# Kernel optimization log

Hardware: AMD Instinct MI355X
Metric: run time of the kernel (lower is better)

## Reference

```python
import jax, jax.numpy as jnp
import numpy as np

THRESHOLD = 0.5


def _crop_resize(img, hstart, ch, wstart, cw, out_h, out_w):
    # Bilinear resample (TF half-pixel-centers) of the crop
    # img[hstart:hstart+ch, wstart:wstart+cw] up to (out_h, out_w).
    chf = ch.astype(jnp.float32)
    cwf = cw.astype(jnp.float32)
    ys = jnp.clip((jnp.arange(out_h, dtype=jnp.float32) + 0.5) * (chf / out_h) - 0.5,
                  0.0, chf - 1.0) + hstart
    xs = jnp.clip((jnp.arange(out_w, dtype=jnp.float32) + 0.5) * (cwf / out_w) - 0.5,
                  0.0, cwf - 1.0) + wstart
    y0 = jnp.floor(ys).astype(jnp.int32)
    y1 = jnp.minimum(y0 + 1, hstart + ch - 1)
    x0 = jnp.floor(xs).astype(jnp.int32)
    x1 = jnp.minimum(x0 + 1, wstart + cw - 1)
    wy = (ys - y0)[:, None, None]
    wx = (xs - x0)[None, :, None]
    r0 = img[y0]  # (out_h, W, C) gathered rows
    r1 = img[y1]
    top = (1.0 - wx) * r0[:, x0] + wx * r0[:, x1]
    bot = (1.0 - wx) * r1[:, x0] + wx * r1[:, x1]
    return (1.0 - wy) * top + wy * bot


def _per_sample(mask, img):
    H, W = img.shape[0], img.shape[1]
    m = (mask >= THRESHOLD).astype(img.dtype)  # (H, W, 1)
    masked = m * img                           # (H, W, C)
    rows = jnp.sum(m[..., 0], axis=1)          # row sums (H,)
    cols = jnp.sum(m[..., 0], axis=0)          # col sums (W,)
    # bbox: first nonzero index - 1 (clamped to 0), last nonzero index + 1
    xl = jnp.maximum(jnp.argmax(rows > 0).astype(jnp.int32) - 1, 0)
    xr = (H - jnp.argmax((rows > 0)[::-1])).astype(jnp.int32)
    yl = jnp.maximum(jnp.argmax(cols > 0).astype(jnp.int32) - 1, 0)
    yr = (W - jnp.argmax((cols > 0)[::-1])).astype(jnp.int32)
    h = xr - xl
    w = yr - yl
    # smart_resize with square target: center-crop bbox to square side min(h, w)
    c = jnp.minimum(h, w)
    hstart = xl + (h - c) // 2
    wstart = yl + (w - c) // 2
    return _crop_resize(masked, hstart, c, wstart, c, H, W)


def setup_inputs() -> dict:
    key = jax.random.key(0)
    k1, k2 = jax.random.split(key)
    masks = jax.random.uniform(k1, (16, 1024, 1024, 1), dtype=jnp.float32)
    images = jax.random.uniform(k2, (16, 1024, 1024, 3), dtype=jnp.float32)
    return {"masks": masks, "images": images}


def reference(masks, images):
    return jax.vmap(_per_sample)(masks, images)
```

## Files before the change

kernel.cpp:

```cpp
#include <hip/hip_runtime.h>

#define HH 1024
#define WW 1024
#define NS 16
#define PR 4
#define RB 4

typedef float f32x4 __attribute__((ext_vector_type(4)));

__global__ __launch_bounds__(256)
void pack_kernel(const float* __restrict__ mask,
                 unsigned int* __restrict__ packed,
                 int* __restrict__ rowMinC,
                 int* __restrict__ rowMaxC) {
    const int s  = blockIdx.y;
    const int r0 = blockIdx.x * PR;
    const int t  = threadIdx.x;

    const f32x4* m4 = (const f32x4*)(mask + (size_t)s * HH * WW);
    __shared__ int smin[PR][4], smax[PR][4];

    for (int rr = 0; rr < PR; ++rr) {
        const int row = r0 + rr;
        f32x4 v = __builtin_nontemporal_load(&m4[(size_t)row * 256 + t]);
        unsigned int w = (v.x >= 0.5f ? 1u : 0u)
                       | (v.y >= 0.5f ? 2u : 0u)
                       | (v.z >= 0.5f ? 4u : 0u)
                       | (v.w >= 0.5f ? 8u : 0u);
        w |= __shfl_down(w, 1) << 4;
        w |= __shfl_down(w, 2) << 8;
        w |= __shfl_down(w, 4) << 16;

        int cmin = WW, cmax = -1;
        if ((t & 7) == 0) {
            int g = t >> 3;
            packed[((size_t)s * HH + row) * 32 + g] = w;
            if (w) {
                cmin = (g << 5) + __builtin_ctz(w);
                cmax = (g << 5) + 31 - __builtin_clz(w);
            }
        }
        for (int off = 32; off > 0; off >>= 1) {
            cmin = min(cmin, __shfl_down(cmin, off));
            cmax = max(cmax, __shfl_down(cmax, off));
        }
        if ((t & 63) == 0) { smin[rr][t >> 6] = cmin; smax[rr][t >> 6] = cmax; }
    }
    __syncthreads();
    if (t < PR) {
        int cmin = min(min(smin[t][0], smin[t][1]), min(smin[t][2], smin[t][3]));
        int cmax = max(max(smax[t][0], smax[t][1]), max(smax[t][2], smax[t][3]));
        rowMinC[s * HH + r0 + t] = cmin;
        rowMaxC[s * HH + r0 + t] = cmax;
    }
}

__global__ __launch_bounds__(256)
void reduce_kernel(const int* __restrict__ rowMinC,
                   const int* __restrict__ rowMaxC,
                   int* __restrict__ bc4) {
    const int s = blockIdx.x;
    const int t = threadIdx.x;
    int minR = HH, maxR = -1, minC = WW, maxC = -1;
#pragma unroll
    for (int m = 0; m < HH / 256; ++m) {
        int r = t + (m << 8);
        int mc = rowMaxC[s * HH + r];
        if (mc >= 0) {
            minR = min(minR, r);
            maxR = max(maxR, r);
            minC = min(minC, rowMinC[s * HH + r]);
            maxC = max(maxC, mc);
        }
    }
    for (int off = 32; off > 0; off >>= 1) {
        minR = min(minR, __shfl_down(minR, off));
        maxR = max(maxR, __shfl_down(maxR, off));
        minC = min(minC, __shfl_down(minC, off));
        maxC = max(maxC, __shfl_down(maxC, off));
    }
    __shared__ int sm[4][4];
    int wave = t >> 6, lane = t & 63;
    if (lane == 0) { sm[wave][0] = minR; sm[wave][1] = maxR; sm[wave][2] = minC; sm[wave][3] = maxC; }
    __syncthreads();
    if (t == 0) {
        for (int wv = 1; wv < 4; ++wv) {
            minR = min(minR, sm[wv][0]);
            maxR = max(maxR, sm[wv][1]);
            minC = min(minC, sm[wv][2]);
            maxC = max(maxC, sm[wv][3]);
        }
        int xl, xr, yl, yr;
        if (maxR < 0) { xl = 0; xr = HH; } else { xl = max(minR - 1, 0); xr = maxR + 1; }
        if (maxC < 0) { yl = 0; yr = WW; } else { yl = max(minC - 1, 0); yr = maxC + 1; }
        int h = xr - xl, w = yr - yl;
        int c = min(h, w);
        bc4[s * 4 + 0] = c;
        bc4[s * 4 + 1] = xl + (h - c) / 2;
        bc4[s * 4 + 2] = yl + (w - c) / 2;
        bc4[s * 4 + 3] = 0;
    }
}

__global__ __launch_bounds__(256)
void resize_kernel(const float* __restrict__ mask,
                   const float* __restrict__ img,
                   const unsigned int* __restrict__ packed,
                   const int* __restrict__ bc4,
                   float* __restrict__ out) {
    const int s  = blockIdx.y;
    const int r0 = blockIdx.x * RB;
    const int t  = threadIdx.x;

    __shared__ unsigned int pw[RB][32];
    if (t < RB * 32) pw[t >> 5][t & 31] = packed[((size_t)s * HH + r0) * 32 + t];

    const int c      = bc4[s * 4 + 0];
    const int hstart = bc4[s * 4 + 1];
    const int wstart = bc4[s * 4 + 2];
    __syncthreads();

    const float* im = img + (size_t)s * HH * WW * 3;
    float*       ob = out + (size_t)s * HH * WW * 3;

    if (c == HH && c == WW && hstart == 0 && wstart == 0) {
        const f32x4* ip = (const f32x4*)(im + (size_t)r0 * WW * 3);
        f32x4*       op = (f32x4*)(ob + (size_t)r0 * WW * 3);
        for (int rr = 0; rr < RB; ++rr) {
            const unsigned int* pwr = pw[rr];
#pragma unroll
            for (int j = 0; j < 3; ++j) {
                int fi = t + (j << 8);
                int F  = fi << 2;
                int p0 = F / 3;
                int r  = F - p0 * 3;
                unsigned int b0 = (pwr[p0 >> 5] >> (p0 & 31)) & 1u;
                int p1 = p0 + 1;
                unsigned int b1 = (pwr[p1 >> 5] >> (p1 & 31)) & 1u;
                size_t off = (size_t)rr * 768 + fi;
                f32x4 v = __builtin_nontemporal_load(&ip[off]);
                f32x4 o;
                o.x = b0 ? v.x : 0.0f;
                o.y = ((r < 2) ? b0 : b1) ? v.y : 0.0f;
                o.z = ((r == 0) ? b0 : b1) ? v.z : 0.0f;
                o.w = b1 ? v.w : 0.0f;
                __builtin_nontemporal_store(o, &op[off]);
            }
        }
        return;
    }

    const float* msk = mask + (size_t)s * HH * WW;
    float cf = (float)c;
    float sy = cf / (float)HH;
    float sx = cf / (float)WW;

    for (int rr = 0; rr < RB; ++rr) {
        const int row = r0 + rr;
        float ysf = fminf(fmaxf((row + 0.5f) * sy - 0.5f, 0.0f), cf - 1.0f);
        int   y0i = (int)floorf(ysf);
        float wy  = ysf - (float)y0i;
        int   ry0 = hstart + y0i;
        int   ry1 = min(ry0 + 1, hstart + c - 1);
        float* orow = ob + (size_t)row * WW * 3;

        for (int k = 0; k < 4; ++k) {
            int ox = (t << 2) + k;
            float xsf = fminf(fmaxf((ox + 0.5f) * sx - 0.5f, 0.0f), cf - 1.0f);
            int   x0i = (int)floorf(xsf);
            float wx  = xsf - (float)x0i;
            int   rx0 = wstart + x0i;
            int   rx1 = min(rx0 + 1, wstart + c - 1);

            float p00[3], p01[3], p10[3], p11[3];
            auto fetch = [&](int y, int x, float* p) {
                int idx = y * WW + x;
                float mv = msk[idx];
                if (mv >= 0.5f) {
                    const float* q = im + (size_t)idx * 3;
                    p[0] = q[0]; p[1] = q[1]; p[2] = q[2];
                } else {
                    p[0] = 0.0f; p[1] = 0.0f; p[2] = 0.0f;
                }
            };
            fetch(ry0, rx0, p00);
            fetch(ry0, rx1, p01);
            fetch(ry1, rx0, p10);
            fetch(ry1, rx1, p11);

            float* o = orow + (size_t)ox * 3;
#pragma unroll
            for (int ch = 0; ch < 3; ++ch) {
                float top = (1.0f - wx) * p00[ch] + wx * p01[ch];
                float bot = (1.0f - wx) * p10[ch] + wx * p11[ch];
                o[ch] = (1.0f - wy) * top + wy * bot;
            }
        }
    }
}

extern "C" void kernel_launch(void* const* d_in, const int* in_sizes, int n_in,
                              void* d_out, int out_size, void* d_ws, size_t ws_size,
                              hipStream_t stream) {
    const float* masks  = (const float*)d_in[0];
    const float* images = (const float*)d_in[1];
    float* out = (float*)d_out;

    int* rowMinC     = (int*)d_ws;
    int* rowMaxC     = rowMinC + NS * HH;
    int* bc4         = rowMaxC + NS * HH;
    unsigned int* pk = (unsigned int*)(bc4 + NS * 4);

    pack_kernel  <<<dim3(HH / PR, NS), 256, 0, stream>>>(masks, pk, rowMinC, rowMaxC);
    reduce_kernel<<<NS,                256, 0, stream>>>(rowMinC, rowMaxC, bc4);
    resize_kernel<<<dim3(HH / RB, NS), 256, 0, stream>>>(masks, images, pk, bc4, out);
}
```

Baseline: 93.03 us.

## Fuse mask packing with speculative identity masked copy, add fixup kernel

```diff
diff --git a/kernel.cpp b/kernel.cpp
--- a/kernel.cpp
+++ b/kernel.cpp
@@ -3,24 +3,25 @@
 #define HH 1024
 #define WW 1024
 #define NS 16
-#define PR 4
 #define RB 4
 
 typedef float f32x4 __attribute__((ext_vector_type(4)));
 
 __global__ __launch_bounds__(256)
-void pack_kernel(const float* __restrict__ mask,
-                 unsigned int* __restrict__ packed,
-                 int* __restrict__ rowMinC,
-                 int* __restrict__ rowMaxC) {
+void fused_kernel(const float* __restrict__ mask,
+                  const float* __restrict__ img,
+                  int* __restrict__ rowMinC,
+                  int* __restrict__ rowMaxC,
+                  float* __restrict__ out) {
     const int s  = blockIdx.y;
-    const int r0 = blockIdx.x * PR;
+    const int r0 = blockIdx.x * RB;
     const int t  = threadIdx.x;
 
     const f32x4* m4 = (const f32x4*)(mask + (size_t)s * HH * WW);
-    __shared__ int smin[PR][4], smax[PR][4];
-
-    for (int rr = 0; rr < PR; ++rr) {
+    __shared__ unsigned int pw[RB][32];
+    __shared__ int smin[RB][4], smax[RB][4];
+
+    for (int rr = 0; rr < RB; ++rr) {
         const int row = r0 + rr;
         f32x4 v = __builtin_nontemporal_load(&m4[(size_t)row * 256 + t]);
         unsigned int w = (v.x >= 0.5f ? 1u : 0u)
@@ -34,7 +35,7 @@
         int cmin = WW, cmax = -1;
         if ((t & 7) == 0) {
             int g = t >> 3;
-            packed[((size_t)s * HH + row) * 32 + g] = w;
+            pw[rr][g] = w;
             if (w) {
                 cmin = (g << 5) + __builtin_ctz(w);
                 cmax = (g << 5) + 31 - __builtin_clz(w);
@@ -47,11 +48,35 @@
         if ((t & 63) == 0) { smin[rr][t >> 6] = cmin; smax[rr][t >> 6] = cmax; }
     }
     __syncthreads();
-    if (t < PR) {
+    if (t < RB) {
         int cmin = min(min(smin[t][0], smin[t][1]), min(smin[t][2], smin[t][3]));
         int cmax = max(max(smax[t][0], smax[t][1]), max(smax[t][2], smax[t][3]));
         rowMinC[s * HH + r0 + t] = cmin;
         rowMaxC[s * HH + r0 + t] = cmax;
+    }
+
+    const f32x4* ip = (const f32x4*)(img + ((size_t)s * HH + r0) * WW * 3);
+    f32x4*       op = (f32x4*)(out + ((size_t)s * HH + r0) * WW * 3);
+    for (int rr = 0; rr < RB; ++rr) {
+        const unsigned int* pwr = pw[rr];
+#pragma unroll
+        for (int j = 0; j < 3; ++j) {
+            int fi = t + (j << 8);
+            int F  = fi << 2;
+            int p0 = F / 3;
+            int r  = F - p0 * 3;
+            unsigned int b0 = (pwr[p0 >> 5] >> (p0 & 31)) & 1u;
+            int p1 = p0 + 1;
+            unsigned int b1 = (pwr[p1 >> 5] >> (p1 & 31)) & 1u;
+            size_t off = (size_t)rr * 768 + fi;
+            f32x4 v = __builtin_nontemporal_load(&ip[off]);
+            f32x4 o;
+            o.x = b0 ? v.x : 0.0f;
+            o.y = ((r < 2) ? b0 : b1) ? v.y : 0.0f;
+            o.z = ((r == 0) ? b0 : b1) ? v.z : 0.0f;
+            o.w = b1 ? v.w : 0.0f;
+            __builtin_nontemporal_store(o, &op[off]);
+        }
     }
 }
 
@@ -103,54 +128,22 @@
 }
 
 __global__ __launch_bounds__(256)
-void resize_kernel(const float* __restrict__ mask,
-                   const float* __restrict__ img,
-                   const unsigned int* __restrict__ packed,
-                   const int* __restrict__ bc4,
-                   float* __restrict__ out) {
+void fixup_kernel(const float* __restrict__ mask,
+                  const float* __restrict__ img,
+                  const int* __restrict__ bc4,
+                  float* __restrict__ out) {
     const int s  = blockIdx.y;
-    const int r0 = blockIdx.x * RB;
-    const int t  = threadIdx.x;
-
-    __shared__ unsigned int pw[RB][32];
-    if (t < RB * 32) pw[t >> 5][t & 31] = packed[((size_t)s * HH + r0) * 32 + t];
-
     const int c      = bc4[s * 4 + 0];
     const int hstart = bc4[s * 4 + 1];
     const int wstart = bc4[s * 4 + 2];
-    __syncthreads();
-
-    const float* im = img + (size_t)s * HH * WW * 3;
-    float*       ob = out + (size_t)s * HH * WW * 3;
-
-    if (c == HH && c == WW && hstart == 0 && wstart == 0) {
-        const f32x4* ip = (const f32x4*)(im + (size_t)r0 * WW * 3);
-        f32x4*       op = (f32x4*)(ob + (size_t)r0 * WW * 3);
-        for (int rr = 0; rr < RB; ++rr) {
-            const unsigned int* pwr = pw[rr];
-#pragma unroll
-            for (int j = 0; j < 3; ++j) {
-                int fi = t + (j << 8);
-                int F  = fi << 2;
-                int p0 = F / 3;
-                int r  = F - p0 * 3;
-                unsigned int b0 = (pwr[p0 >> 5] >> (p0 & 31)) & 1u;
-                int p1 = p0 + 1;
-                unsigned int b1 = (pwr[p1 >> 5] >> (p1 & 31)) & 1u;
-                size_t off = (size_t)rr * 768 + fi;
-                f32x4 v = __builtin_nontemporal_load(&ip[off]);
-                f32x4 o;
-                o.x = b0 ? v.x : 0.0f;
-                o.y = ((r < 2) ? b0 : b1) ? v.y : 0.0f;
-                o.z = ((r == 0) ? b0 : b1) ? v.z : 0.0f;
-                o.w = b1 ? v.w : 0.0f;
-                __builtin_nontemporal_store(o, &op[off]);
-            }
-        }
-        return;
-    }
-
+    if (c == HH && hstart == 0 && wstart == 0) return;
+
+    const int r0 = blockIdx.x * RB;
+    const int t  = threadIdx.x;
     const float* msk = mask + (size_t)s * HH * WW;
+    const float* im  = img  + (size_t)s * HH * WW * 3;
+    float*       ob  = out  + (size_t)s * HH * WW * 3;
+
     float cf = (float)c;
     float sy = cf / (float)HH;
     float sx = cf / (float)WW;
@@ -206,12 +199,11 @@
     const float* images = (const float*)d_in[1];
     float* out = (float*)d_out;
 
-    int* rowMinC     = (int*)d_ws;
-    int* rowMaxC     = rowMinC + NS * HH;
-    int* bc4         = rowMaxC + NS * HH;
-    unsigned int* pk = (unsigned int*)(bc4 + NS * 4);
-
-    pack_kernel  <<<dim3(HH / PR, NS), 256, 0, stream>>>(masks, pk, rowMinC, rowMaxC);
+    int* rowMinC = (int*)d_ws;
+    int* rowMaxC = rowMinC + NS * HH;
+    int* bc4     = rowMaxC + NS * HH;
+
+    fused_kernel <<<dim3(HH / RB, NS), 256, 0, stream>>>(masks, images, rowMinC, rowMaxC, out);
     reduce_kernel<<<NS,                256, 0, stream>>>(rowMinC, rowMaxC, bc4);
-    resize_kernel<<<dim3(HH / RB, NS), 256, 0, stream>>>(masks, images, pk, bc4, out);
-}
+    fixup_kernel <<<dim3(HH / RB, NS), 256, 0, stream>>>(masks, images, bc4, out);
+}
```

Result: faster. 88.88 us (-4.5%).
